# Kernel optimization log

Measured on AMD Instinct MI355X. Metric: run time of the kernel, lower is better.

The kernel has to match this reference:

```python
import jax, jax.numpy as jnp
import numpy as np

DIM = 192
NUM_HEADS = 6
HEAD_DIM = DIM // NUM_HEADS
WS = 8            # window_size
SHIFT = 4         # shift_size
SCALE = HEAD_DIM ** -0.5


def window_partition(x, ws):
    # x: (B, H, W, C) -> (B*nWh*nWw, ws, ws, C)
    B, H, W, C = x.shape
    x = x.reshape(B, H // ws, ws, W // ws, ws, C)
    x = x.transpose(0, 1, 3, 2, 4, 5)
    return x.reshape(-1, ws, ws, C)


def window_reverse(windows, ws, H, W):
    C = windows.shape[-1]
    B = windows.shape[0] // ((H // ws) * (W // ws))
    x = windows.reshape(B, H // ws, W // ws, ws, ws, C)
    x = x.transpose(0, 1, 3, 2, 4, 5)
    return x.reshape(B, H, W, C)


def depthwise_conv3x3(x, w, b):
    # x: (N, H, W, C), w: (3, 3, 1, C) HWIO with feature_group_count=C
    y = jax.lax.conv_general_dilated(
        x, w, window_strides=(1, 1), padding='SAME',
        dimension_numbers=('NHWC', 'HWIO', 'NHWC'),
        feature_group_count=x.shape[-1])
    return y + b


def setup_inputs() -> dict:
    key = jax.random.key(0)
    ks = jax.random.split(key, 5)
    B, H, W = 4, 128, 128
    WB = B * (H // WS) * (W // WS)  # 1024 windows
    N = WS * WS                      # 64 tokens per window
    x = jax.random.normal(ks[0], (B, H, W, DIM), dtype=jnp.float32)
    prev_attn_map = jax.random.uniform(ks[1], (WB, NUM_HEADS, N, N), dtype=jnp.float32)
    qkv_w = jax.random.normal(ks[2], (DIM, 3 * DIM), dtype=jnp.float32) * 0.02
    qkv_b = jnp.zeros((3 * DIM,), dtype=jnp.float32)
    proj_w = jax.random.normal(ks[3], (DIM, DIM), dtype=jnp.float32) * 0.02
    proj_b = jnp.zeros((DIM,), dtype=jnp.float32)
    lepe_w = jax.random.normal(ks[4], (3, 3, 1, DIM), dtype=jnp.float32) * 0.02
    lepe_b = jnp.zeros((DIM,), dtype=jnp.float32)
    return {'x': x, 'prev_attn_map': prev_attn_map, 'qkv_w': qkv_w, 'qkv_b': qkv_b,
            'proj_w': proj_w, 'proj_b': proj_b, 'lepe_w': lepe_w, 'lepe_b': lepe_b}


def reference(x, prev_attn_map, qkv_w, qkv_b, proj_w, proj_b, lepe_w, lepe_b):
    B, H, W, C = x.shape
    N = WS * WS
    # shifted window partition
    shifted = jnp.roll(x, shift=(-SHIFT, -SHIFT), axis=(1, 2))
    xw = window_partition(shifted, WS)              # (WB, ws, ws, C)
    WB = xw.shape[0]
    xw = xw.reshape(WB, N, C)
    # QKV projection
    qkv = xw @ qkv_w + qkv_b                        # (WB, N, 3C)
    qkv = qkv.reshape(WB, N, 3, NUM_HEADS, HEAD_DIM).transpose(2, 0, 3, 1, 4)
    q, k, v = qkv[0], qkv[1], qkv[2]                # (WB, nh, N, hd)
    # LePE: depthwise conv on v in 2D window layout
    v_2d = v.transpose(0, 2, 1, 3).reshape(WB, WS, WS, C)
    lepe_v = depthwise_conv3x3(v_2d, lepe_w, lepe_b)
    lepe_v = lepe_v.reshape(WB, N, NUM_HEADS, HEAD_DIM).transpose(0, 2, 1, 3)
    v = v + lepe_v
    # attention with inherited-map Hadamard gating
    attn_scores = jnp.einsum('bhqd,bhkd->bhqk', q, k) * SCALE
    attn_scores = attn_scores * prev_attn_map       # progressive focusing
    attn = jax.nn.softmax(attn_scores, axis=-1)     # (WB, nh, N, N)
    out = jnp.einsum('bhqk,bhkd->bhqd', attn, v)
    out = out.transpose(0, 2, 1, 3).reshape(WB, N, C)
    out = out @ proj_w + proj_b
    # reverse windows and unshift
    out = window_reverse(out.reshape(WB, WS, WS, C), WS, H, W)
    out = jnp.roll(out, shift=(SHIFT, SHIFT), axis=(1, 2))
    return out, attn
```

## Files before the change

### kernel.cpp

```cpp
#include <hip/hip_runtime.h>


#define SCALE 0.17677669529663687f

typedef __attribute__((ext_vector_type(8))) short short8;
typedef __attribute__((ext_vector_type(4))) float f32x4;

__device__ __forceinline__ unsigned short f2bf(float f) {
    unsigned int u = __float_as_uint(f);
    u = (u + 0x7FFFu + ((u >> 16) & 1u)) >> 16;
    return (unsigned short)u;
}
__device__ __forceinline__ float bf2f(unsigned short h) {
    return __uint_as_float(((unsigned int)h) << 16);
}
__device__ __forceinline__ unsigned int pack2(float a, float b) {
    return (unsigned int)f2bf(a) | ((unsigned int)f2bf(b) << 16);
}

__global__ __launch_bounds__(256) void k0_pack(const float* __restrict__ qkv_w,
                                               const float* __restrict__ proj_w,
                                               unsigned short* __restrict__ qkvp,
                                               unsigned short* __restrict__ projp) {
    int gid = blockIdx.x * 256 + threadIdx.x;
    if (gid < 6 * 36 * 64) {
        int lane = gid & 63, tile = gid >> 6;
        int nt = tile % 36, ks = tile / 36;
        int row = ks * 32 + (lane >> 4) * 8, col = nt * 16 + (lane & 15);
        const float* w = qkv_w + (size_t)row * 576 + col;
        uint4 o;
        o.x = pack2(w[0 * 576], w[1 * 576]);
        o.y = pack2(w[2 * 576], w[3 * 576]);
        o.z = pack2(w[4 * 576], w[5 * 576]);
        o.w = pack2(w[6 * 576], w[7 * 576]);
        *(uint4*)(qkvp + (size_t)gid * 8) = o;
    } else {
        int g = gid - 6 * 36 * 64;
        int lane = g & 63, tile = g >> 6;
        int nt = tile % 12, ks = tile / 12;
        int row = ks * 32 + (lane >> 4) * 8, col = nt * 16 + (lane & 15);
        const float* w = proj_w + (size_t)row * 192 + col;
        uint4 o;
        o.x = pack2(w[0 * 192], w[1 * 192]);
        o.y = pack2(w[2 * 192], w[3 * 192]);
        o.z = pack2(w[4 * 192], w[5 * 192]);
        o.w = pack2(w[6 * 192], w[7 * 192]);
        *(uint4*)(projp + (size_t)g * 8) = o;
    }
}

#define RH 4352
#define KO 2048
#define PO 2304
#define WREG 26112

__global__ __launch_bounds__(768, 3) void k_fused(
    const float* __restrict__ x, const float* __restrict__ prev,
    const float* __restrict__ qkv_b, const float* __restrict__ lepe_w,
    const float* __restrict__ lepe_b, const float* __restrict__ proj_b,
    const unsigned short* __restrict__ qkvp, const unsigned short* __restrict__ projp,
    float* __restrict__ out, float* __restrict__ attn)
{
    __shared__ unsigned short lds[2 * WREG + 7680];
    const int t = threadIdx.x;
    const int win = (t >= 384) ? 1 : 0;
    const int tl = t - win * 384;
    const int wb = blockIdx.x * 2 + win;
    const int b = wb >> 8, wh = (wb >> 4) & 15, wwi = wb & 15;
    const int lane = tl & 63, h = tl >> 6, quad = lane >> 4, l16 = lane & 15;
    unsigned short* ldsw = &lds[win * WREG];
    const f32x4 fz = {0.f, 0.f, 0.f, 0.f};

    float* lw = (float*)(lds + 2 * WREG) + (win * 6 + h) * 320;
    for (int i = lane; i < 320; i += 64) {
        float v = (i < 288) ? lepe_w[(i >> 5) * 192 + h * 32 + (i & 31)]
                            : lepe_b[h * 32 + (i - 288)];
        lw[i] = v;
    }

#pragma unroll
    for (int kk = 0; kk < 8; ++kk) {
        int f = kk * 384 + tl;
        int token = f / 48, c4 = f - token * 48;
        int i = token >> 3, j = token & 7;
        int hh = (wh * 8 + i + 4) & 127, wp = (wwi * 8 + j + 4) & 127;
        const float4 v4 = *(const float4*)(x + ((size_t)((b * 128 + hh) * 128 + wp)) * 192 + c4 * 4);
        unsigned int* d = (unsigned int*)&ldsw[token * 200 + c4 * 4];
        d[0] = pack2(v4.x, v4.y);
        d[1] = pack2(v4.z, v4.w);
    }
    __syncthreads();

    const int ntg[6] = {2 * h, 2 * h + 1, 12 + 2 * h, 13 + 2 * h, 24 + 2 * h, 25 + 2 * h};
    unsigned short* qh  = ldsw + h * RH;
    unsigned short* kh  = qh + KO;
    unsigned short* vth = qh;
    unsigned short* Pf  = qh + PO;

    unsigned int qpk[4][4], kpk[4][4], vpk[4][4];

#pragma unroll
    for (int pass = 0; pass < 3; ++pass) {
        f32x4 a2[2][4];
#pragma unroll
        for (int jj = 0; jj < 2; ++jj)
#pragma unroll
            for (int m = 0; m < 4; ++m) a2[jj][m] = fz;

#pragma unroll
        for (int ks = 0; ks < 6; ++ks) {
            short8 a[4];
#pragma unroll
            for (int m = 0; m < 4; ++m)
                a[m] = *(const short8*)&ldsw[(m * 16 + l16) * 200 + ks * 32 + quad * 8];
            __builtin_amdgcn_s_setprio(1);
#pragma unroll
            for (int jj = 0; jj < 2; ++jj) {
                short8 bf = *(const short8*)(qkvp +
                    (((size_t)(ks * 36 + ntg[pass * 2 + jj]) * 64 + lane) << 3));
#pragma unroll
                for (int m = 0; m < 4; ++m)
                    a2[jj][m] = __builtin_amdgcn_mfma_f32_16x16x32_bf16(a[m], bf, a2[jj][m], 0, 0, 0);
            }
            __builtin_amdgcn_s_setprio(0);
        }
        float b0 = qkv_b[ntg[pass * 2] * 16 + l16];
        float b1 = qkv_b[ntg[pass * 2 + 1] * 16 + l16];
#pragma unroll
        for (int m = 0; m < 4; ++m)
#pragma unroll
            for (int r = 0; r < 4; ++r) {
                unsigned int pk = pack2(a2[0][m][r] + b0, a2[1][m][r] + b1);
                if (pass == 0)      qpk[m][r] = pk;
                else if (pass == 1) kpk[m][r] = pk;
                else                vpk[m][r] = pk;
            }
    }
    __syncthreads();

#pragma unroll
    for (int m = 0; m < 4; ++m)
#pragma unroll
        for (int r = 0; r < 4; ++r) {
            int token = m * 16 + quad * 4 + r;
            unsigned int uq = qpk[m][r], uk = kpk[m][r];
            qh[token * 32 + l16]      = (unsigned short)(uq & 0xFFFFu);
            qh[token * 32 + 16 + l16] = (unsigned short)(uq >> 16);
            kh[token * 32 + l16]      = (unsigned short)(uk & 0xFFFFu);
            kh[token * 32 + 16 + l16] = (unsigned short)(uk >> 16);
        }

    f32x4 s4[4][4];
    {
        short8 aq[4];
#pragma unroll
        for (int m = 0; m < 4; ++m)
            aq[m] = *(const short8*)(qh + (m * 16 + l16) * 32 + quad * 8);
        __builtin_amdgcn_s_setprio(1);
#pragma unroll
        for (int nt = 0; nt < 4; ++nt) {
            short8 bk = *(const short8*)(kh + (nt * 16 + l16) * 32 + quad * 8);
#pragma unroll
            for (int m = 0; m < 4; ++m)
                s4[m][nt] = __builtin_amdgcn_mfma_f32_16x16x32_bf16(aq[m], bk, fz, 0, 0, 0);
        }
        __builtin_amdgcn_s_setprio(0);
    }

#pragma unroll
    for (int m = 0; m < 4; ++m)
#pragma unroll
        for (int r = 0; r < 4; ++r) {
            int token = m * 16 + quad * 4 + r;
            unsigned int uv = vpk[m][r];
            vth[l16 * 72 + token]        = (unsigned short)(uv & 0xFFFFu);
            vth[(16 + l16) * 72 + token] = (unsigned short)(uv >> 16);
        }

    {
        const int ti = lane >> 3, tj = lane & 7;
#pragma unroll 8
        for (int ci = 0; ci < 32; ++ci) {
            const unsigned short* vr = vth + ci * 72;
            float sum = bf2f(vr[lane]) + lw[288 + ci];
#pragma unroll
            for (int di = -1; di <= 1; ++di)
#pragma unroll
                for (int dj = -1; dj <= 1; ++dj) {
                    int ii = ti + di, jj = tj + dj;
                    if (ii >= 0 && ii < 8 && jj >= 0 && jj < 8)
                        sum += bf2f(vr[ii * 8 + jj]) * lw[((di + 1) * 3 + (dj + 1)) * 32 + ci];
                }
            vth[ci * 72 + lane] = f2bf(sum);
        }
    }

    const float* pvm = prev + (((size_t)wb * 6 + h) << 12);
    float* aom = attn + (((size_t)wb * 6 + h) << 12);
#pragma unroll
    for (int m = 0; m < 4; ++m) {
        float inv[4];
#pragma unroll
        for (int r = 0; r < 4; ++r) {
            int row = m * 16 + quad * 4 + r;
            float ps = 0.f;
#pragma unroll
            for (int nt = 0; nt < 4; ++nt) {
                float sg = s4[m][nt][r] * SCALE * pvm[row * 64 + nt * 16 + l16];
                float ev = __expf(sg);
                s4[m][nt][r] = ev; ps += ev;
            }
            ps += __shfl_xor(ps, 1); ps += __shfl_xor(ps, 2);
            ps += __shfl_xor(ps, 4); ps += __shfl_xor(ps, 8);
            inv[r] = 1.0f / ps;
        }
#pragma unroll
        for (int r = 0; r < 4; ++r) {
            int row = m * 16 + quad * 4 + r;
#pragma unroll
            for (int nt = 0; nt < 4; ++nt) {
                float av = s4[m][nt][r] * inv[r];
                s4[m][nt][r] = av;
                aom[row * 64 + nt * 16 + l16] = av;
            }
        }
    }

    {
        f32x4 o2[4][2];
#pragma unroll
        for (int m = 0; m < 4; ++m) { o2[m][0] = fz; o2[m][1] = fz; }
#pragma unroll
        for (int half = 0; half < 2; ++half) {
#pragma unroll
            for (int m = 0; m < 4; ++m)
#pragma unroll
                for (int nt2 = 0; nt2 < 2; ++nt2)
#pragma unroll
                    for (int r = 0; r < 4; ++r) {
                        int row = m * 16 + quad * 4 + r;
                        Pf[row * 32 + nt2 * 16 + l16] = f2bf(s4[m][half * 2 + nt2][r]);
                    }
            short8 ap[4];
#pragma unroll
            for (int m = 0; m < 4; ++m)
                ap[m] = *(const short8*)(Pf + (m * 16 + l16) * 32 + quad * 8);
            __builtin_amdgcn_s_setprio(1);
#pragma unroll
            for (int n2 = 0; n2 < 2; ++n2) {
                short8 bv = *(const short8*)(vth + (n2 * 16 + l16) * 72 + half * 32 + quad * 8);
#pragma unroll
                for (int m = 0; m < 4; ++m)
                    o2[m][n2] = __builtin_amdgcn_mfma_f32_16x16x32_bf16(ap[m], bv, o2[m][n2], 0, 0, 0);
            }
            __builtin_amdgcn_s_setprio(0);
        }
#pragma unroll
        for (int m = 0; m < 4; ++m)
#pragma unroll
            for (int n2 = 0; n2 < 2; ++n2)
#pragma unroll
                for (int r = 0; r < 4; ++r) {
                    int token = m * 16 + quad * 4 + r;
                    Pf[token * 32 + n2 * 16 + l16] = f2bf(o2[m][n2][r]);
                }
    }
    __syncthreads();

    {
        f32x4 p3[2][4];
#pragma unroll
        for (int n = 0; n < 2; ++n)
#pragma unroll
            for (int m = 0; m < 4; ++m) p3[n][m] = fz;

#pragma unroll
        for (int ks = 0; ks < 6; ++ks) {
            const unsigned short* ob = ldsw + ks * RH + PO;
            short8 a3[4];
#pragma unroll
            for (int m = 0; m < 4; ++m)
                a3[m] = *(const short8*)(ob + (m * 16 + l16) * 32 + quad * 8);
            __builtin_amdgcn_s_setprio(1);
#pragma unroll
            for (int n = 0; n < 2; ++n) {
                short8 bf = *(const short8*)(projp + (((size_t)(ks * 12 + h * 2 + n) * 64 + lane) << 3));
#pragma unroll
                for (int m = 0; m < 4; ++m)
                    p3[n][m] = __builtin_amdgcn_mfma_f32_16x16x32_bf16(a3[m], bf, p3[n][m], 0, 0, 0);
            }
            __builtin_amdgcn_s_setprio(0);
        }
#pragma unroll
        for (int n = 0; n < 2; ++n) {
            int col = (h * 2 + n) * 16 + l16;
            float bias = proj_b[col];
#pragma unroll
            for (int m = 0; m < 4; ++m)
#pragma unroll
                for (int r = 0; r < 4; ++r) {
                    int token = m * 16 + quad * 4 + r;
                    int i = token >> 3, j = token & 7;
                    int hh = (wh * 8 + i + 4) & 127, wp = (wwi * 8 + j + 4) & 127;
                    out[((size_t)((b * 128 + hh) * 128 + wp)) * 192 + col] = p3[n][m][r] + bias;
                }
        }
    }
}

extern "C" void kernel_launch(void* const* d_in, const int* in_sizes, int n_in,
                              void* d_out, int out_size, void* d_ws, size_t ws_size,
                              hipStream_t stream) {
    const float* x      = (const float*)d_in[0];
    const float* prev   = (const float*)d_in[1];
    const float* qkv_w  = (const float*)d_in[2];
    const float* qkv_b  = (const float*)d_in[3];
    const float* proj_w = (const float*)d_in[4];
    const float* proj_b = (const float*)d_in[5];
    const float* lepe_w = (const float*)d_in[6];
    const float* lepe_b = (const float*)d_in[7];

    float* out  = (float*)d_out;
    float* attn = out + (size_t)4 * 128 * 128 * 192;

    char* ws = (char*)d_ws;
    const size_t SZ_QKVP = 192 * 576 * 2;
    unsigned short* qkvp  = (unsigned short*)(ws);
    unsigned short* projp = (unsigned short*)(ws + SZ_QKVP);

    k0_pack<<<72, 256, 0, stream>>>(qkv_w, proj_w, qkvp, projp);
    k_fused<<<512, 768, 0, stream>>>(x, prev, qkv_b, lepe_w, lepe_b, proj_b,
                                     qkvp, projp, out, attn);
}
```

Baseline: 332.5 us.

## Separate x-window LDS region from per-head Q/K buffers to drop register staging

Gives the staged input window its own LDS region, separate from the per-head Q/K/P scratch, so Q and K can be written straight to LDS right after each projection pass. This removes the qpk/kpk register arrays and one block barrier. The LePE weights are now loaded once per block and shared by both windows. Total LDS grows from about 120 KB to 160 KB, which may lower how many blocks fit per CU, in exchange for lower register pressure.

```diff
diff --git a/kernel.cpp b/kernel.cpp
--- a/kernel.cpp
+++ b/kernel.cpp
@@ -49,10 +49,12 @@
     }
 }
 
+#define XWP 12800
+#define HREG 25600
 #define RH 4352
 #define KO 2048
 #define PO 2304
-#define WREG 26112
+#define LEPE 77824
 
 __global__ __launch_bounds__(768, 3) void k_fused(
     const float* __restrict__ x, const float* __restrict__ prev,
@@ -61,21 +63,23 @@
     const unsigned short* __restrict__ qkvp, const unsigned short* __restrict__ projp,
     float* __restrict__ out, float* __restrict__ attn)
 {
-    __shared__ unsigned short lds[2 * WREG + 7680];
+    __shared__ unsigned short lds[81664];
     const int t = threadIdx.x;
     const int win = (t >= 384) ? 1 : 0;
     const int tl = t - win * 384;
     const int wb = blockIdx.x * 2 + win;
     const int b = wb >> 8, wh = (wb >> 4) & 15, wwi = wb & 15;
     const int lane = tl & 63, h = tl >> 6, quad = lane >> 4, l16 = lane & 15;
-    unsigned short* ldsw = &lds[win * WREG];
+    unsigned short* xww = &lds[win * XWP];
     const f32x4 fz = {0.f, 0.f, 0.f, 0.f};
 
-    float* lw = (float*)(lds + 2 * WREG) + (win * 6 + h) * 320;
-    for (int i = lane; i < 320; i += 64) {
-        float v = (i < 288) ? lepe_w[(i >> 5) * 192 + h * 32 + (i & 31)]
-                            : lepe_b[h * 32 + (i - 288)];
-        lw[i] = v;
+    float* lw = (float*)&lds[LEPE] + h * 320;
+    if (win == 0) {
+        for (int i = lane; i < 320; i += 64) {
+            float v = (i < 288) ? lepe_w[(i >> 5) * 192 + h * 32 + (i & 31)]
+                                : lepe_b[h * 32 + (i - 288)];
+            lw[i] = v;
+        }
     }
 
 #pragma unroll
@@ -85,19 +89,19 @@
         int i = token >> 3, j = token & 7;
         int hh = (wh * 8 + i + 4) & 127, wp = (wwi * 8 + j + 4) & 127;
         const float4 v4 = *(const float4*)(x + ((size_t)((b * 128 + hh) * 128 + wp)) * 192 + c4 * 4);
-        unsigned int* d = (unsigned int*)&ldsw[token * 200 + c4 * 4];
+        unsigned int* d = (unsigned int*)&xww[token * 200 + c4 * 4];
         d[0] = pack2(v4.x, v4.y);
         d[1] = pack2(v4.z, v4.w);
     }
     __syncthreads();
 
     const int ntg[6] = {2 * h, 2 * h + 1, 12 + 2 * h, 13 + 2 * h, 24 + 2 * h, 25 + 2 * h};
-    unsigned short* qh  = ldsw + h * RH;
+    unsigned short* qh  = &lds[HREG + (win * 6 + h) * RH];
     unsigned short* kh  = qh + KO;
     unsigned short* vth = qh;
     unsigned short* Pf  = qh + PO;
 
-    unsigned int qpk[4][4], kpk[4][4], vpk[4][4];
+    unsigned int vpk[4][4];
 
 #pragma unroll
     for (int pass = 0; pass < 3; ++pass) {
@@ -112,7 +116,7 @@
             short8 a[4];
 #pragma unroll
             for (int m = 0; m < 4; ++m)
-                a[m] = *(const short8*)&ldsw[(m * 16 + l16) * 200 + ks * 32 + quad * 8];
+                a[m] = *(const short8*)&xww[(m * 16 + l16) * 200 + ks * 32 + quad * 8];
             __builtin_amdgcn_s_setprio(1);
 #pragma unroll
             for (int jj = 0; jj < 2; ++jj) {
@@ -126,29 +130,24 @@
         }
         float b0 = qkv_b[ntg[pass * 2] * 16 + l16];
         float b1 = qkv_b[ntg[pass * 2 + 1] * 16 + l16];
-#pragma unroll
-        for (int m = 0; m < 4; ++m)
-#pragma unroll
-            for (int r = 0; r < 4; ++r) {
-                unsigned int pk = pack2(a2[0][m][r] + b0, a2[1][m][r] + b1);
-                if (pass == 0)      qpk[m][r] = pk;
-                else if (pass == 1) kpk[m][r] = pk;
-                else                vpk[m][r] = pk;
-            }
-    }
-    __syncthreads();
-
-#pragma unroll
-    for (int m = 0; m < 4; ++m)
-#pragma unroll
-        for (int r = 0; r < 4; ++r) {
-            int token = m * 16 + quad * 4 + r;
-            unsigned int uq = qpk[m][r], uk = kpk[m][r];
-            qh[token * 32 + l16]      = (unsigned short)(uq & 0xFFFFu);
-            qh[token * 32 + 16 + l16] = (unsigned short)(uq >> 16);
-            kh[token * 32 + l16]      = (unsigned short)(uk & 0xFFFFu);
-            kh[token * 32 + 16 + l16] = (unsigned short)(uk >> 16);
-        }
+        if (pass < 2) {
+            unsigned short* base = (pass == 0) ? qh : kh;
+#pragma unroll
+            for (int m = 0; m < 4; ++m)
+#pragma unroll
+                for (int r = 0; r < 4; ++r) {
+                    int token = m * 16 + quad * 4 + r;
+                    base[token * 32 + l16]      = f2bf(a2[0][m][r] + b0);
+                    base[token * 32 + 16 + l16] = f2bf(a2[1][m][r] + b1);
+                }
+        } else {
+#pragma unroll
+            for (int m = 0; m < 4; ++m)
+#pragma unroll
+                for (int r = 0; r < 4; ++r)
+                    vpk[m][r] = pack2(a2[0][m][r] + b0, a2[1][m][r] + b1);
+        }
+    }
 
     f32x4 s4[4][4];
     {
@@ -276,7 +275,7 @@
 
 #pragma unroll
         for (int ks = 0; ks < 6; ++ks) {
-            const unsigned short* ob = ldsw + ks * RH + PO;
+            const unsigned short* ob = &lds[HREG + (win * 6 + ks) * RH + PO];
             short8 a3[4];
 #pragma unroll
             for (int m = 0; m < 4; ++m)
```

Measured after the change: 321.6 us (median of 2 runs). -3.3%, faster.
